# Optimization experiments

Measured on AMD Instinct MI355X. Metric: run time of the kernel, lower is better.

## Reference

```python
import jax, jax.numpy as jnp
import numpy as np

N_NODES = 100000
N_EDGES = 1600000
N_GRAPHS = 256
K_HOPS = 3


def setup_inputs() -> dict:
    key = jax.random.key(0)
    ks = jax.random.split(key, 10)
    x = jax.random.normal(ks[0], (N_NODES, 32), dtype=jnp.float32)
    edge_index = jax.random.randint(ks[1], (2, N_EDGES), 0, N_NODES, dtype=jnp.int32)
    batch = jnp.sort(jax.random.randint(ks[2], (N_NODES,), 0, N_GRAPHS, dtype=jnp.int32))
    gcn_w = jax.random.normal(ks[3], (64, 32), dtype=jnp.float32) * 0.1
    gcn_b = jax.random.normal(ks[4], (64,), dtype=jnp.float32) * 0.1
    w1 = jax.random.normal(ks[5], (32, 64), dtype=jnp.float32) * 0.1
    b1 = jax.random.normal(ks[6], (32,), dtype=jnp.float32) * 0.1
    w2 = jax.random.normal(ks[7], (16, 32), dtype=jnp.float32) * 0.1
    b2 = jax.random.normal(ks[8], (16,), dtype=jnp.float32) * 0.1
    return {"x": x, "edge_index": edge_index, "batch": batch,
            "gcn_w": gcn_w, "gcn_b": gcn_b, "w1": w1, "b1": b1, "w2": w2, "b2": b2}


def reference(x, edge_index, batch, gcn_w, gcn_b, w1, b1, w2, b2):
    N = x.shape[0]
    src, dst = edge_index[0], edge_index[1]
    # GCN symmetric normalization with self-loops: deg = in-degree + 1
    deg = jax.ops.segment_sum(jnp.ones_like(src, dtype=x.dtype), dst, num_segments=N) + 1.0
    norm = deg ** -0.5  # [N]
    h = x
    for _ in range(K_HOPS):
        # edge message: norm[src] * h[src], scattered to dst, scaled by norm[dst];
        # self-loop contributes norm[i]^2 * h[i]
        msg = h[src] * norm[src][:, None]                     # [E, C]
        agg = jax.ops.segment_sum(msg, dst, num_segments=N)    # [N, C]
        h = norm[:, None] * agg + (norm * norm)[:, None] * h
    h = jax.nn.relu(h @ gcn_w.T + gcn_b)                       # [N, hidden]
    # global mean pool per graph
    counts = jax.ops.segment_sum(jnp.ones((N,), x.dtype), batch, num_segments=N_GRAPHS)
    sums = jax.ops.segment_sum(h, batch, num_segments=N_GRAPHS)
    h_avg = sums / jnp.maximum(counts, 1.0)[:, None]           # [G, hidden]
    # classifier (dropout = identity in eval)
    h1 = jax.nn.relu(h_avg @ w1.T + b1)
    logits = h1 @ w2.T + b2                                    # [G, nc]
    return logits
```

## Files before the change

### kernel.cpp

```cpp
#include <hip/hip_runtime.h>

constexpr int NW    = 391;
constexpr int CH    = 8192;
constexpr int CAP_B = 8192;
constexpr int CAP_C = 10240;

__device__ __forceinline__ unsigned bf16_rne(float x) {
    unsigned u = __float_as_uint(x);
    u += 0x7fffu + ((u >> 16) & 1u);
    return u >> 16;
}
__device__ __forceinline__ unsigned pack2(float even, float odd) {
    return bf16_rne(even) | (bf16_rne(odd) << 16);
}
__device__ __forceinline__ float lo_f(unsigned u) { return __uint_as_float(u << 16); }
__device__ __forceinline__ float hi_f(unsigned u) { return __uint_as_float(u & 0xffff0000u); }


__global__ __launch_bounds__(512) void k_bucket(const int* __restrict__ src,
                                                const int* __restrict__ dst, int E,
                                                int* __restrict__ wcur, int* __restrict__ packed) {
    __shared__ int h[256];
    __shared__ int base[256];
    int t = threadIdx.x;
    if (t < 256) h[t] = 0;
    __syncthreads();
    int b0 = blockIdx.x * CH;
    int cnt = min(CH, E - b0);
    if (cnt == CH) {
        const int4* d4 = (const int4*)(dst + b0);
        for (int i = t; i < CH / 4; i += 512) {
            int4 v = d4[i];
            atomicAdd(&h[v.x / NW], 1); atomicAdd(&h[v.y / NW], 1);
            atomicAdd(&h[v.z / NW], 1); atomicAdd(&h[v.w / NW], 1);
        }
    } else {
        for (int i = t; i < cnt; i += 512) atomicAdd(&h[dst[b0 + i] / NW], 1);
    }
    __syncthreads();
    if (t < 256) { base[t] = atomicAdd(&wcur[t], h[t]); h[t] = 0; }
    __syncthreads();
    if (cnt == CH) {
        const int4* d4 = (const int4*)(dst + b0);
        const int4* s4 = (const int4*)(src + b0);
        for (int i = t; i < CH / 4; i += 512) {
            int4 dv = d4[i];
            int4 sv = s4[i];
            int da[4] = {dv.x, dv.y, dv.z, dv.w};
            int sa[4] = {sv.x, sv.y, sv.z, sv.w};
#pragma unroll
            for (int j = 0; j < 4; ++j) {
                int w = da[j] / NW;
                int l = da[j] - w * NW;
                int r = atomicAdd(&h[w], 1);
                int pos = base[w] + r;
                if (pos < CAP_B) packed[w * CAP_B + pos] = (l << 17) | sa[j];
            }
        }
    } else {
        for (int i = t; i < cnt; i += 512) {
            int d = dst[b0 + i];
            int s = src[b0 + i];
            int w = d / NW;
            int l = d - w * NW;
            int r = atomicAdd(&h[w], 1);
            int pos = base[w] + r;
            if (pos < CAP_B) packed[w * CAP_B + pos] = (l << 17) | s;
        }
    }
}


__global__ __launch_bounds__(512) void k_window(const int* __restrict__ packed,
                                                const int* __restrict__ wcur,
                                                const float4* __restrict__ x4,
                                                float* __restrict__ norm,
                                                int2* __restrict__ rng,
                                                int* __restrict__ csr,
                                                uint2* __restrict__ hb, int N, int W) {
    __shared__ int hist[NW];
    __shared__ float snorm[NW];
    __shared__ int pend[NW];
    __shared__ int cur[NW];
    __shared__ int wpart[8];
    int t = threadIdx.x, w = blockIdx.x;
    int lo = w * NW, nwn = min(NW, N - lo);
    for (int i = t; i < NW; i += 512) hist[i] = 0;
    __syncthreads();
    int cnt = min(wcur[w], CAP_B);
    const int* pk = packed + (size_t)w * CAP_B;
    for (int e = t; e < cnt; e += 512) atomicAdd(&hist[pk[e] >> 17], 1);
    __syncthreads();
    int d = (t < nwn) ? hist[t] : 0;
    float nv = rsqrtf((float)(d + 1));
    if (t < nwn) { snorm[t] = nv; norm[lo + t] = nv; }
    int pd = (t < nwn) ? ((d + 7) & ~7) : 0;
    int lane = t & 63, wid = t >> 6;
    int v = pd;
#pragma unroll
    for (int s = 1; s < 64; s <<= 1) {
        int u = __shfl_up(v, s, 64);
        if (lane >= s) v += u;
    }
    if (lane == 63) wpart[wid] = v;
    __syncthreads();
    if (t < 8) {
        int z = wpart[t];
#pragma unroll
        for (int s = 1; s < 8; s <<= 1) {
            int u = __shfl_up(z, s, 8);
            if (t >= s) z += u;
        }
        wpart[t] = z;
    }
    __syncthreads();
    int incl = v + (wid ? wpart[wid - 1] : 0);
    int base = w * CAP_C;
    int cend = base + incl;
    if (t < nwn) {
        rng[lo + t] = make_int2(cend - pd, cend);
        pend[t] = cend;
        cur[t] = cend - pd;
    }
    if (w == W - 1 && t == 0) { norm[N] = 1.f; rng[N] = make_int2(0, 0); }
    __syncthreads();
    for (int e = t; e < cnt; e += 512) {
        int p = pk[e];
        int pos = atomicAdd(&cur[p >> 17], 1);
        csr[pos] = p & 0x1FFFF;
    }
    __syncthreads();
    if (t < nwn) {
        for (int pos = cur[t]; pos < pend[t]; ++pos) csr[pos] = N;
    }
    for (int idx = t; idx < nwn * 8; idx += 512) {
        int node = idx >> 3, q = idx & 7;
        float nn = snorm[node];
        float4 vx = x4[(size_t)(lo + node) * 8 + q];
        hb[(size_t)(lo + node) * 8 + q] =
            make_uint2(pack2(vx.x * nn, vx.y * nn), pack2(vx.z * nn, vx.w * nn));
    }
    if (w == W - 1 && t < 8) hb[(size_t)N * 8 + t] = make_uint2(0u, 0u);
}

__global__ void k_hop(const uint2* __restrict__ tab, const float* __restrict__ norm,
                      const int2* __restrict__ rng, const int* __restrict__ csr,
                      uint2* __restrict__ outb, int N) {
    int group = (blockIdx.x * blockDim.x + threadIdx.x) >> 3;
    int l = threadIdx.x & 7;
    if (group > N) return;
    uint2 sv = tab[(size_t)group * 8 + l];
    float ax = lo_f(sv.x), ay = hi_f(sv.x), az = lo_f(sv.y), aw = hi_f(sv.y);
    int2 be = rng[group];
    int k = be.x;
    for (; k + 16 <= be.y; k += 16) {
        int e0 = csr[k + l];
        int e1 = csr[k + 8 + l];
        uint2 u[16];
#pragma unroll
        for (int j = 0; j < 8; ++j) {
            int s = __shfl(e0, j, 8);
            u[j] = tab[(size_t)s * 8 + l];
        }
#pragma unroll
        for (int j = 0; j < 8; ++j) {
            int s = __shfl(e1, j, 8);
            u[8 + j] = tab[(size_t)s * 8 + l];
        }
#pragma unroll
        for (int j = 0; j < 16; ++j) {
            ax += lo_f(u[j].x); ay += hi_f(u[j].x);
            az += lo_f(u[j].y); aw += hi_f(u[j].y);
        }
    }
    if (k < be.y) {
        int e = csr[k + l];
        uint2 u[8];
#pragma unroll
        for (int j = 0; j < 8; ++j) {
            int s = __shfl(e, j, 8);
            u[j] = tab[(size_t)s * 8 + l];
        }
#pragma unroll
        for (int j = 0; j < 8; ++j) {
            ax += lo_f(u[j].x); ay += hi_f(u[j].x);
            az += lo_f(u[j].y); aw += hi_f(u[j].y);
        }
    }
    float n = norm[group];
    float sc = n * n;
    outb[(size_t)group * 8 + l] = make_uint2(pack2(ax * sc, ay * sc), pack2(az * sc, aw * sc));
}

__global__ __launch_bounds__(256) void k_hopfeat(const uint2* __restrict__ tab,
                                                 const float* __restrict__ norm,
                                                 const int2* __restrict__ rng,
                                                 const int* __restrict__ csr,
                                                 const float* __restrict__ gw,
                                                 const float* __restrict__ gb,
                                                 uint4* __restrict__ zb4, int N) {
    __shared__ float wT[32][64];
    __shared__ float bs[64];
    __shared__ float rows[32][33];
    int t = threadIdx.x;
    for (int i = t; i < 64 * 32; i += 256) { int c = i >> 5, k = i & 31; wT[k][c] = gw[i]; }
    if (t < 64) bs[t] = gb[t];
    int group = (blockIdx.x * 256 + t) >> 3;
    int l = t & 7;
    int node = t >> 3;
    float ax = 0.f, ay = 0.f, az = 0.f, aw = 0.f;
    if (group <= N) {
        uint2 sv = tab[(size_t)group * 8 + l];
        ax = lo_f(sv.x); ay = hi_f(sv.x); az = lo_f(sv.y); aw = hi_f(sv.y);
        int2 be = rng[group];
        int k = be.x;
        for (; k + 16 <= be.y; k += 16) {
            int e0 = csr[k + l];
            int e1 = csr[k + 8 + l];
            uint2 u[16];
#pragma unroll
            for (int j = 0; j < 8; ++j) {
                int s = __shfl(e0, j, 8);
                u[j] = tab[(size_t)s * 8 + l];
            }
#pragma unroll
            for (int j = 0; j < 8; ++j) {
                int s = __shfl(e1, j, 8);
                u[8 + j] = tab[(size_t)s * 8 + l];
            }
#pragma unroll
            for (int j = 0; j < 16; ++j) {
                ax += lo_f(u[j].x); ay += hi_f(u[j].x);
                az += lo_f(u[j].y); aw += hi_f(u[j].y);
            }
        }
        if (k < be.y) {
            int e = csr[k + l];
            uint2 u[8];
#pragma unroll
            for (int j = 0; j < 8; ++j) {
                int s = __shfl(e, j, 8);
                u[j] = tab[(size_t)s * 8 + l];
            }
#pragma unroll
            for (int j = 0; j < 8; ++j) {
                ax += lo_f(u[j].x); ay += hi_f(u[j].x);
                az += lo_f(u[j].y); aw += hi_f(u[j].y);
            }
        }
        float n = norm[group];
        ax *= n; ay *= n; az *= n; aw *= n;
    }
    rows[node][l * 4 + 0] = ax;
    rows[node][l * 4 + 1] = ay;
    rows[node][l * 4 + 2] = az;
    rows[node][l * 4 + 3] = aw;
    __syncthreads();
    if (group < N) {
        int c0 = l * 8;
        float o[8];
#pragma unroll
        for (int cc = 0; cc < 8; ++cc) {
            float d = bs[c0 + cc];
#pragma unroll
            for (int k = 0; k < 32; ++k) d += rows[node][k] * wT[k][c0 + cc];
            o[cc] = fmaxf(d, 0.f);
        }
        zb4[(size_t)group * 8 + l] =
            make_uint4(pack2(o[0], o[1]), pack2(o[2], o[3]), pack2(o[4], o[5]), pack2(o[6], o[7]));
    }
}


__global__ __launch_bounds__(256) void k_pool(const uint2* __restrict__ zb2,
                                              const int* __restrict__ batch, int N,
                                              const float* __restrict__ w1, const float* __restrict__ b1,
                                              const float* __restrict__ w2, const float* __restrict__ b2,
                                              float* __restrict__ out) {
    __shared__ float4 part[16][17];
    __shared__ float havg[64];
    __shared__ float h1s[32];
    __shared__ int se[2];
    int t = threadIdx.x, g = blockIdx.x;
    if (t < 2) {
        int target = g + t;
        int lo = 0, hi = N;
        while (lo < hi) { int mid = (lo + hi) >> 1; if (batch[mid] < target) lo = mid + 1; else hi = mid; }
        se[t] = lo;
    }
    __syncthreads();
    int start = se[0], end = se[1];
    int q = t & 15;
    int r = t >> 4;
    float4 acc = make_float4(0.f, 0.f, 0.f, 0.f);
    for (int n = start + r; n < end; n += 16) {
        uint2 v = zb2[(size_t)n * 16 + q];
        acc.x += lo_f(v.x); acc.y += hi_f(v.x); acc.z += lo_f(v.y); acc.w += hi_f(v.y);
    }
    part[r][q] = acc;
    __syncthreads();
#pragma unroll
    for (int s = 8; s > 0; s >>= 1) {
        if (r < s) {
            float4 a = part[r][q], b = part[r + s][q];
            a.x += b.x; a.y += b.y; a.z += b.z; a.w += b.w;
            part[r][q] = a;
        }
        __syncthreads();
    }
    if (t < 16) {
        int cnt = end - start;
        float inv = 1.f / (float)(cnt > 0 ? cnt : 1);
        float4 a = part[0][t];
        havg[t * 4] = a.x * inv; havg[t * 4 + 1] = a.y * inv;
        havg[t * 4 + 2] = a.z * inv; havg[t * 4 + 3] = a.w * inv;
    }
    __syncthreads();
    if (t < 32) {
        float d = b1[t];
#pragma unroll
        for (int k = 0; k < 64; ++k) d += havg[k] * w1[t * 64 + k];
        h1s[t] = fmaxf(d, 0.f);
    }
    __syncthreads();
    if (t < 16) {
        float d = b2[t];
#pragma unroll
        for (int j = 0; j < 32; ++j) d += h1s[j] * w2[t * 32 + j];
        out[g * 16 + t] = d;
    }
}


extern "C" void kernel_launch(void* const* d_in, const int* in_sizes, int n_in,
                              void* d_out, int out_size, void* d_ws, size_t ws_size,
                              hipStream_t stream) {
    const float* x     = (const float*)d_in[0];
    const int*   ei    = (const int*)d_in[1];
    const int*   batch = (const int*)d_in[2];
    const float* gw    = (const float*)d_in[3];
    const float* gb    = (const float*)d_in[4];
    const float* w1    = (const float*)d_in[5];
    const float* b1    = (const float*)d_in[6];
    const float* w2    = (const float*)d_in[7];
    const float* b2    = (const float*)d_in[8];
    float* out = (float*)d_out;

    int N = in_sizes[2];
    int E = in_sizes[1] / 2;
    int G = out_size / 16;
    const int* srcp = ei;
    const int* dstp = ei + E;

    int W  = (N + NW - 1) / NW;
    int NB = (E + CH - 1) / CH;

    char* ws = (char*)d_ws;
    size_t off = 0;
    auto alloc = [&](size_t bytes) -> void* {
        void* p = ws + off;
        off += (bytes + 255) & ~(size_t)255;
        return p;
    };
    int*   wcur   = (int*)alloc(256 * 4);
    int*   packed = (int*)alloc((size_t)W * CAP_B * 4);
    int*   csr    = (int*)alloc((size_t)W * CAP_C * 4);
    int2*  rng    = (int2*)alloc((size_t)(N + 1) * 8);
    float* norm   = (float*)alloc((size_t)(N + 1) * 4);
    uint2* hbA    = (uint2*)alloc((size_t)(N + 1) * 64);
    uint2* hbB    = (uint2*)alloc((size_t)(N + 1) * 64);
    unsigned* zbuf = (unsigned*)alloc((size_t)N * 64 * 2);

    hipMemsetAsync(wcur, 0, 256 * 4, stream);

    int pb = ((N + 1) * 8 + 255) / 256;

    k_bucket<<<NB, 512, 0, stream>>>(srcp, dstp, E, wcur, packed);
    k_window<<<W, 512, 0, stream>>>(packed, wcur, (const float4*)x, norm, rng, csr, hbA, N, W);

    k_hop<<<pb, 256, 0, stream>>>(hbA, norm, rng, csr, hbB, N);
    k_hop<<<pb, 256, 0, stream>>>(hbB, norm, rng, csr, hbA, N);
    k_hopfeat<<<pb, 256, 0, stream>>>(hbA, norm, rng, csr, gw, gb, (uint4*)zbuf, N);

    k_pool<<<G, 256, 0, stream>>>((const uint2*)zbuf, batch, N, w1, b1, w2, b2, out);
}
```

Before: 203.0 us.

## Fuse all GCN stages into one persistent cooperative kernel with grid syncs

Replaces the six separate kernel launches with a single cooperative persistent kernel that runs bucket, window/CSR build, two hops, hop+feature and pool phases separated by grid.sync, and keeps the multi-launch path as a fallback. Window size, chunk size and block size are halved (NW 196, 256 threads) so each window fits a 256-thread block and more windows give better load balance. The aim is to remove launch gaps and tail effects between the small stages. In exchange the grid is capped at 1024 blocks with grid-stride loops, which may reduce latency hiding in the gather-heavy hop phases, and grid barriers add their own cost.

```diff
diff --git a/kernel.cpp b/kernel.cpp
--- a/kernel.cpp
+++ b/kernel.cpp
@@ -1,9 +1,13 @@
 #include <hip/hip_runtime.h>
-
-constexpr int NW    = 391;
-constexpr int CH    = 8192;
-constexpr int CAP_B = 8192;
-constexpr int CAP_C = 10240;
+#include <hip/hip_cooperative_groups.h>
+
+namespace cg = cooperative_groups;
+
+constexpr int NW    = 196;
+constexpr int CH    = 3200;
+constexpr int CAP_B = 4096;
+constexpr int CAP_C = 5632;
+constexpr int NTHR  = 256;
 
 __device__ __forceinline__ unsigned bf16_rne(float x) {
     unsigned u = __float_as_uint(x);
@@ -16,202 +20,150 @@
 __device__ __forceinline__ float lo_f(unsigned u) { return __uint_as_float(u << 16); }
 __device__ __forceinline__ float hi_f(unsigned u) { return __uint_as_float(u & 0xffff0000u); }
 
-
-__global__ __launch_bounds__(512) void k_bucket(const int* __restrict__ src,
-                                                const int* __restrict__ dst, int E,
-                                                int* __restrict__ wcur, int* __restrict__ packed) {
-    __shared__ int h[256];
-    __shared__ int base[256];
+struct KParams {
+    const int* src; const int* dst; int E;
+    int* wcur; int* packed;
+    const float4* x4; float* norm; int2* rng; int* csr;
+    uint2* hbA; uint2* hbB; uint4* zb4;
+    const int* batch; const float* gw; const float* gb;
+    const float* w1; const float* b1; const float* w2; const float* b2;
+    float* out; int N; int W; int NB; int G;
+};
+
+union SharedU {
+    struct { int h[512]; int base[512]; } bk;
+    struct { int hist[NW]; float snorm[NW]; int pend[NW]; int cur[NW]; int wpart[8]; } wd;
+    struct { float wT[32][64]; float bs[64]; float rows[32][33]; } ft;
+    struct { float4 part[16][17]; float havg[64]; float h1s[32]; int se[2]; } pl;
+};
+
+__device__ void phase_bucket(const KParams& p, SharedU& su) {
     int t = threadIdx.x;
-    if (t < 256) h[t] = 0;
-    __syncthreads();
-    int b0 = blockIdx.x * CH;
-    int cnt = min(CH, E - b0);
-    if (cnt == CH) {
-        const int4* d4 = (const int4*)(dst + b0);
-        for (int i = t; i < CH / 4; i += 512) {
-            int4 v = d4[i];
-            atomicAdd(&h[v.x / NW], 1); atomicAdd(&h[v.y / NW], 1);
-            atomicAdd(&h[v.z / NW], 1); atomicAdd(&h[v.w / NW], 1);
-        }
-    } else {
-        for (int i = t; i < cnt; i += 512) atomicAdd(&h[dst[b0 + i] / NW], 1);
-    }
-    __syncthreads();
-    if (t < 256) { base[t] = atomicAdd(&wcur[t], h[t]); h[t] = 0; }
-    __syncthreads();
-    if (cnt == CH) {
-        const int4* d4 = (const int4*)(dst + b0);
-        const int4* s4 = (const int4*)(src + b0);
-        for (int i = t; i < CH / 4; i += 512) {
-            int4 dv = d4[i];
-            int4 sv = s4[i];
-            int da[4] = {dv.x, dv.y, dv.z, dv.w};
-            int sa[4] = {sv.x, sv.y, sv.z, sv.w};
-#pragma unroll
-            for (int j = 0; j < 4; ++j) {
-                int w = da[j] / NW;
-                int l = da[j] - w * NW;
-                int r = atomicAdd(&h[w], 1);
-                int pos = base[w] + r;
-                if (pos < CAP_B) packed[w * CAP_B + pos] = (l << 17) | sa[j];
-            }
-        }
-    } else {
-        for (int i = t; i < cnt; i += 512) {
-            int d = dst[b0 + i];
-            int s = src[b0 + i];
-            int w = d / NW;
-            int l = d - w * NW;
-            int r = atomicAdd(&h[w], 1);
-            int pos = base[w] + r;
-            if (pos < CAP_B) packed[w * CAP_B + pos] = (l << 17) | s;
-        }
-    }
-}
-
-
-__global__ __launch_bounds__(512) void k_window(const int* __restrict__ packed,
-                                                const int* __restrict__ wcur,
-                                                const float4* __restrict__ x4,
-                                                float* __restrict__ norm,
-                                                int2* __restrict__ rng,
-                                                int* __restrict__ csr,
-                                                uint2* __restrict__ hb, int N, int W) {
-    __shared__ int hist[NW];
-    __shared__ float snorm[NW];
-    __shared__ int pend[NW];
-    __shared__ int cur[NW];
-    __shared__ int wpart[8];
-    int t = threadIdx.x, w = blockIdx.x;
-    int lo = w * NW, nwn = min(NW, N - lo);
-    for (int i = t; i < NW; i += 512) hist[i] = 0;
-    __syncthreads();
-    int cnt = min(wcur[w], CAP_B);
-    const int* pk = packed + (size_t)w * CAP_B;
-    for (int e = t; e < cnt; e += 512) atomicAdd(&hist[pk[e] >> 17], 1);
-    __syncthreads();
-    int d = (t < nwn) ? hist[t] : 0;
-    float nv = rsqrtf((float)(d + 1));
-    if (t < nwn) { snorm[t] = nv; norm[lo + t] = nv; }
-    int pd = (t < nwn) ? ((d + 7) & ~7) : 0;
-    int lane = t & 63, wid = t >> 6;
-    int v = pd;
-#pragma unroll
-    for (int s = 1; s < 64; s <<= 1) {
-        int u = __shfl_up(v, s, 64);
-        if (lane >= s) v += u;
-    }
-    if (lane == 63) wpart[wid] = v;
-    __syncthreads();
-    if (t < 8) {
-        int z = wpart[t];
-#pragma unroll
-        for (int s = 1; s < 8; s <<= 1) {
-            int u = __shfl_up(z, s, 8);
-            if (t >= s) z += u;
-        }
-        wpart[t] = z;
-    }
-    __syncthreads();
-    int incl = v + (wid ? wpart[wid - 1] : 0);
-    int base = w * CAP_C;
-    int cend = base + incl;
-    if (t < nwn) {
-        rng[lo + t] = make_int2(cend - pd, cend);
-        pend[t] = cend;
-        cur[t] = cend - pd;
-    }
-    if (w == W - 1 && t == 0) { norm[N] = 1.f; rng[N] = make_int2(0, 0); }
-    __syncthreads();
-    for (int e = t; e < cnt; e += 512) {
-        int p = pk[e];
-        int pos = atomicAdd(&cur[p >> 17], 1);
-        csr[pos] = p & 0x1FFFF;
-    }
-    __syncthreads();
-    if (t < nwn) {
-        for (int pos = cur[t]; pos < pend[t]; ++pos) csr[pos] = N;
-    }
-    for (int idx = t; idx < nwn * 8; idx += 512) {
-        int node = idx >> 3, q = idx & 7;
-        float nn = snorm[node];
-        float4 vx = x4[(size_t)(lo + node) * 8 + q];
-        hb[(size_t)(lo + node) * 8 + q] =
-            make_uint2(pack2(vx.x * nn, vx.y * nn), pack2(vx.z * nn, vx.w * nn));
-    }
-    if (w == W - 1 && t < 8) hb[(size_t)N * 8 + t] = make_uint2(0u, 0u);
-}
-
-__global__ void k_hop(const uint2* __restrict__ tab, const float* __restrict__ norm,
-                      const int2* __restrict__ rng, const int* __restrict__ csr,
-                      uint2* __restrict__ outb, int N) {
-    int group = (blockIdx.x * blockDim.x + threadIdx.x) >> 3;
-    int l = threadIdx.x & 7;
-    if (group > N) return;
-    uint2 sv = tab[(size_t)group * 8 + l];
-    float ax = lo_f(sv.x), ay = hi_f(sv.x), az = lo_f(sv.y), aw = hi_f(sv.y);
-    int2 be = rng[group];
-    int k = be.x;
-    for (; k + 16 <= be.y; k += 16) {
-        int e0 = csr[k + l];
-        int e1 = csr[k + 8 + l];
-        uint2 u[16];
-#pragma unroll
-        for (int j = 0; j < 8; ++j) {
-            int s = __shfl(e0, j, 8);
-            u[j] = tab[(size_t)s * 8 + l];
-        }
-#pragma unroll
-        for (int j = 0; j < 8; ++j) {
-            int s = __shfl(e1, j, 8);
-            u[8 + j] = tab[(size_t)s * 8 + l];
-        }
-#pragma unroll
-        for (int j = 0; j < 16; ++j) {
-            ax += lo_f(u[j].x); ay += hi_f(u[j].x);
-            az += lo_f(u[j].y); aw += hi_f(u[j].y);
-        }
-    }
-    if (k < be.y) {
-        int e = csr[k + l];
-        uint2 u[8];
-#pragma unroll
-        for (int j = 0; j < 8; ++j) {
-            int s = __shfl(e, j, 8);
-            u[j] = tab[(size_t)s * 8 + l];
-        }
-#pragma unroll
-        for (int j = 0; j < 8; ++j) {
-            ax += lo_f(u[j].x); ay += hi_f(u[j].x);
-            az += lo_f(u[j].y); aw += hi_f(u[j].y);
-        }
-    }
-    float n = norm[group];
-    float sc = n * n;
-    outb[(size_t)group * 8 + l] = make_uint2(pack2(ax * sc, ay * sc), pack2(az * sc, aw * sc));
-}
-
-__global__ __launch_bounds__(256) void k_hopfeat(const uint2* __restrict__ tab,
-                                                 const float* __restrict__ norm,
-                                                 const int2* __restrict__ rng,
-                                                 const int* __restrict__ csr,
-                                                 const float* __restrict__ gw,
-                                                 const float* __restrict__ gb,
-                                                 uint4* __restrict__ zb4, int N) {
-    __shared__ float wT[32][64];
-    __shared__ float bs[64];
-    __shared__ float rows[32][33];
+    for (int c = blockIdx.x; c < p.NB; c += gridDim.x) {
+        for (int i = t; i < 512; i += NTHR) su.bk.h[i] = 0;
+        __syncthreads();
+        int b0 = c * CH;
+        int cnt = min(CH, p.E - b0);
+        if (cnt == CH) {
+            const int4* d4 = (const int4*)(p.dst + b0);
+            for (int i = t; i < CH / 4; i += NTHR) {
+                int4 v = d4[i];
+                atomicAdd(&su.bk.h[v.x / NW], 1); atomicAdd(&su.bk.h[v.y / NW], 1);
+                atomicAdd(&su.bk.h[v.z / NW], 1); atomicAdd(&su.bk.h[v.w / NW], 1);
+            }
+        } else {
+            for (int i = t; i < cnt; i += NTHR) atomicAdd(&su.bk.h[p.dst[b0 + i] / NW], 1);
+        }
+        __syncthreads();
+        for (int i = t; i < 512; i += NTHR) {
+            su.bk.base[i] = (i < p.W && su.bk.h[i] > 0) ? atomicAdd(&p.wcur[i], su.bk.h[i]) : 0;
+            su.bk.h[i] = 0;
+        }
+        __syncthreads();
+        if (cnt == CH) {
+            const int4* d4 = (const int4*)(p.dst + b0);
+            const int4* s4 = (const int4*)(p.src + b0);
+            for (int i = t; i < CH / 4; i += NTHR) {
+                int4 dv = d4[i];
+                int4 sv = s4[i];
+                int da[4] = {dv.x, dv.y, dv.z, dv.w};
+                int sa[4] = {sv.x, sv.y, sv.z, sv.w};
+#pragma unroll
+                for (int j = 0; j < 4; ++j) {
+                    int w = da[j] / NW;
+                    int l = da[j] - w * NW;
+                    int r = atomicAdd(&su.bk.h[w], 1);
+                    int pos = su.bk.base[w] + r;
+                    if (pos < CAP_B) p.packed[w * CAP_B + pos] = (l << 17) | sa[j];
+                }
+            }
+        } else {
+            for (int i = t; i < cnt; i += NTHR) {
+                int d = p.dst[b0 + i];
+                int s = p.src[b0 + i];
+                int w = d / NW;
+                int l = d - w * NW;
+                int r = atomicAdd(&su.bk.h[w], 1);
+                int pos = su.bk.base[w] + r;
+                if (pos < CAP_B) p.packed[w * CAP_B + pos] = (l << 17) | s;
+            }
+        }
+        __syncthreads();
+    }
+}
+
+__device__ void phase_window(const KParams& p, SharedU& su) {
     int t = threadIdx.x;
-    for (int i = t; i < 64 * 32; i += 256) { int c = i >> 5, k = i & 31; wT[k][c] = gw[i]; }
-    if (t < 64) bs[t] = gb[t];
-    int group = (blockIdx.x * 256 + t) >> 3;
-    int l = t & 7;
-    int node = t >> 3;
-    float ax = 0.f, ay = 0.f, az = 0.f, aw = 0.f;
-    if (group <= N) {
+    for (int w = blockIdx.x; w < p.W; w += gridDim.x) {
+        int lo = w * NW, nwn = min(NW, p.N - lo);
+        for (int i = t; i < NW; i += NTHR) su.wd.hist[i] = 0;
+        __syncthreads();
+        int cnt = min(p.wcur[w], CAP_B);
+        const int* pk = p.packed + (size_t)w * CAP_B;
+        for (int e = t; e < cnt; e += NTHR) atomicAdd(&su.wd.hist[pk[e] >> 17], 1);
+        __syncthreads();
+        int d = (t < nwn) ? su.wd.hist[t] : 0;
+        float nv = rsqrtf((float)(d + 1));
+        if (t < nwn) { su.wd.snorm[t] = nv; p.norm[lo + t] = nv; }
+        int pd = (t < nwn) ? ((d + 7) & ~7) : 0;
+        int lane = t & 63, wid = t >> 6;
+        int v = pd;
+#pragma unroll
+        for (int s = 1; s < 64; s <<= 1) {
+            int u = __shfl_up(v, s, 64);
+            if (lane >= s) v += u;
+        }
+        if (lane == 63) su.wd.wpart[wid] = v;
+        __syncthreads();
+        if (t < 4) {
+            int z = su.wd.wpart[t];
+#pragma unroll
+            for (int s = 1; s < 4; s <<= 1) {
+                int u = __shfl_up(z, s, 4);
+                if (t >= s) z += u;
+            }
+            su.wd.wpart[t] = z;
+        }
+        __syncthreads();
+        int incl = v + (wid ? su.wd.wpart[wid - 1] : 0);
+        int cend = w * CAP_C + incl;
+        if (t < nwn) {
+            p.rng[lo + t] = make_int2(cend - pd, cend);
+            su.wd.pend[t] = cend;
+            su.wd.cur[t] = cend - pd;
+        }
+        if (w == p.W - 1 && t == 0) { p.norm[p.N] = 1.f; p.rng[p.N] = make_int2(0, 0); }
+        __syncthreads();
+        for (int e = t; e < cnt; e += NTHR) {
+            int pp = pk[e];
+            int pos = atomicAdd(&su.wd.cur[pp >> 17], 1);
+            p.csr[pos] = pp & 0x1FFFF;
+        }
+        __syncthreads();
+        if (t < nwn) {
+            for (int pos = su.wd.cur[t]; pos < su.wd.pend[t]; ++pos) p.csr[pos] = p.N;
+        }
+        for (int idx = t; idx < nwn * 8; idx += NTHR) {
+            int node = idx >> 3, q = idx & 7;
+            float nn = su.wd.snorm[node];
+            float4 vx = p.x4[(size_t)(lo + node) * 8 + q];
+            p.hbA[(size_t)(lo + node) * 8 + q] =
+                make_uint2(pack2(vx.x * nn, vx.y * nn), pack2(vx.z * nn, vx.w * nn));
+        }
+        if (w == p.W - 1 && t < 8) p.hbA[(size_t)p.N * 8 + t] = make_uint2(0u, 0u);
+        __syncthreads();
+    }
+}
+
+__device__ void hop_phase(const uint2* __restrict__ tab, const float* __restrict__ norm,
+                          const int2* __restrict__ rng, const int* __restrict__ csr,
+                          uint2* __restrict__ outb, int N) {
+    int stride = gridDim.x * blockDim.x;
+    int total = (N + 1) * 8;
+    for (int idx = blockIdx.x * blockDim.x + threadIdx.x; idx < total; idx += stride) {
+        int group = idx >> 3, l = idx & 7;
         uint2 sv = tab[(size_t)group * 8 + l];
-        ax = lo_f(sv.x); ay = hi_f(sv.x); az = lo_f(sv.y); aw = hi_f(sv.y);
+        float ax = lo_f(sv.x), ay = hi_f(sv.x), az = lo_f(sv.y), aw = hi_f(sv.y);
         int2 be = rng[group];
         int k = be.x;
         for (; k + 16 <= be.y; k += 16) {
@@ -249,138 +201,229 @@
             }
         }
         float n = norm[group];
-        ax *= n; ay *= n; az *= n; aw *= n;
-    }
-    rows[node][l * 4 + 0] = ax;
-    rows[node][l * 4 + 1] = ay;
-    rows[node][l * 4 + 2] = az;
-    rows[node][l * 4 + 3] = aw;
-    __syncthreads();
-    if (group < N) {
-        int c0 = l * 8;
-        float o[8];
-#pragma unroll
-        for (int cc = 0; cc < 8; ++cc) {
-            float d = bs[c0 + cc];
-#pragma unroll
-            for (int k = 0; k < 32; ++k) d += rows[node][k] * wT[k][c0 + cc];
-            o[cc] = fmaxf(d, 0.f);
-        }
-        zb4[(size_t)group * 8 + l] =
-            make_uint4(pack2(o[0], o[1]), pack2(o[2], o[3]), pack2(o[4], o[5]), pack2(o[6], o[7]));
-    }
-}
-
-
-__global__ __launch_bounds__(256) void k_pool(const uint2* __restrict__ zb2,
-                                              const int* __restrict__ batch, int N,
-                                              const float* __restrict__ w1, const float* __restrict__ b1,
-                                              const float* __restrict__ w2, const float* __restrict__ b2,
-                                              float* __restrict__ out) {
-    __shared__ float4 part[16][17];
-    __shared__ float havg[64];
-    __shared__ float h1s[32];
-    __shared__ int se[2];
-    int t = threadIdx.x, g = blockIdx.x;
-    if (t < 2) {
-        int target = g + t;
-        int lo = 0, hi = N;
-        while (lo < hi) { int mid = (lo + hi) >> 1; if (batch[mid] < target) lo = mid + 1; else hi = mid; }
-        se[t] = lo;
-    }
-    __syncthreads();
-    int start = se[0], end = se[1];
-    int q = t & 15;
-    int r = t >> 4;
-    float4 acc = make_float4(0.f, 0.f, 0.f, 0.f);
-    for (int n = start + r; n < end; n += 16) {
-        uint2 v = zb2[(size_t)n * 16 + q];
-        acc.x += lo_f(v.x); acc.y += hi_f(v.x); acc.z += lo_f(v.y); acc.w += hi_f(v.y);
-    }
-    part[r][q] = acc;
-    __syncthreads();
-#pragma unroll
-    for (int s = 8; s > 0; s >>= 1) {
-        if (r < s) {
-            float4 a = part[r][q], b = part[r + s][q];
-            a.x += b.x; a.y += b.y; a.z += b.z; a.w += b.w;
-            part[r][q] = a;
-        }
-        __syncthreads();
-    }
-    if (t < 16) {
-        int cnt = end - start;
-        float inv = 1.f / (float)(cnt > 0 ? cnt : 1);
-        float4 a = part[0][t];
-        havg[t * 4] = a.x * inv; havg[t * 4 + 1] = a.y * inv;
-        havg[t * 4 + 2] = a.z * inv; havg[t * 4 + 3] = a.w * inv;
-    }
-    __syncthreads();
-    if (t < 32) {
-        float d = b1[t];
-#pragma unroll
-        for (int k = 0; k < 64; ++k) d += havg[k] * w1[t * 64 + k];
-        h1s[t] = fmaxf(d, 0.f);
-    }
-    __syncthreads();
-    if (t < 16) {
-        float d = b2[t];
-#pragma unroll
-        for (int j = 0; j < 32; ++j) d += h1s[j] * w2[t * 32 + j];
-        out[g * 16 + t] = d;
-    }
-}
+        float sc = n * n;
+        outb[(size_t)group * 8 + l] = make_uint2(pack2(ax * sc, ay * sc), pack2(az * sc, aw * sc));
+    }
+}
+
+__device__ void phase_hopfeat(const KParams& p, SharedU& su) {
+    int t = threadIdx.x;
+    for (int i = t; i < 64 * 32; i += NTHR) { int c = i >> 5, k = i & 31; su.ft.wT[k][c] = p.gw[i]; }
+    if (t < 64) su.ft.bs[t] = p.gb[t];
+    int stride = gridDim.x * blockDim.x;
+    int total = (p.N + 1) * 8;
+    int node = t >> 3, l = t & 7;
+    for (int base = blockIdx.x * blockDim.x; base < total; base += stride) {
+        int idx = base + t;
+        int group = idx >> 3;
+        float ax = 0.f, ay = 0.f, az = 0.f, aw = 0.f;
+        if (idx < total) {
+            uint2 sv = p.hbA[(size_t)group * 8 + l];
+            ax = lo_f(sv.x); ay = hi_f(sv.x); az = lo_f(sv.y); aw = hi_f(sv.y);
+            int2 be = p.rng[group];
+            int k = be.x;
+            for (; k + 16 <= be.y; k += 16) {
+                int e0 = p.csr[k + l];
+                int e1 = p.csr[k + 8 + l];
+                uint2 u[16];
+#pragma unroll
+                for (int j = 0; j < 8; ++j) {
+                    int s = __shfl(e0, j, 8);
+                    u[j] = p.hbA[(size_t)s * 8 + l];
+                }
+#pragma unroll
+                for (int j = 0; j < 8; ++j) {
+                    int s = __shfl(e1, j, 8);
+                    u[8 + j] = p.hbA[(size_t)s * 8 + l];
+                }
+#pragma unroll
+                for (int j = 0; j < 16; ++j) {
+                    ax += lo_f(u[j].x); ay += hi_f(u[j].x);
+                    az += lo_f(u[j].y); aw += hi_f(u[j].y);
+                }
+            }
+            if (k < be.y) {
+                int e = p.csr[k + l];
+                uint2 u[8];
+#pragma unroll
+                for (int j = 0; j < 8; ++j) {
+                    int s = __shfl(e, j, 8);
+                    u[j] = p.hbA[(size_t)s * 8 + l];
+                }
+#pragma unroll
+                for (int j = 0; j < 8; ++j) {
+                    ax += lo_f(u[j].x); ay += hi_f(u[j].x);
+                    az += lo_f(u[j].y); aw += hi_f(u[j].y);
+                }
+            }
+            float n = p.norm[group];
+            ax *= n; ay *= n; az *= n; aw *= n;
+        }
+        su.ft.rows[node][l * 4 + 0] = ax;
+        su.ft.rows[node][l * 4 + 1] = ay;
+        su.ft.rows[node][l * 4 + 2] = az;
+        su.ft.rows[node][l * 4 + 3] = aw;
+        __syncthreads();
+        if (idx < total && group < p.N) {
+            int c0 = l * 8;
+            float o[8];
+#pragma unroll
+            for (int cc = 0; cc < 8; ++cc) {
+                float dd = su.ft.bs[c0 + cc];
+#pragma unroll
+                for (int k = 0; k < 32; ++k) dd += su.ft.rows[node][k] * su.ft.wT[k][c0 + cc];
+                o[cc] = fmaxf(dd, 0.f);
+            }
+            p.zb4[(size_t)group * 8 + l] = make_uint4(pack2(o[0], o[1]), pack2(o[2], o[3]),
+                                                      pack2(o[4], o[5]), pack2(o[6], o[7]));
+        }
+        __syncthreads();
+    }
+}
+
+__device__ void phase_pool(const KParams& p, SharedU& su) {
+    int t = threadIdx.x;
+    const uint2* zb2 = (const uint2*)p.zb4;
+    for (int g = blockIdx.x; g < p.G; g += gridDim.x) {
+        if (t < 2) {
+            int target = g + t;
+            int lo = 0, hi = p.N;
+            while (lo < hi) { int mid = (lo + hi) >> 1; if (p.batch[mid] < target) lo = mid + 1; else hi = mid; }
+            su.pl.se[t] = lo;
+        }
+        __syncthreads();
+        int start = su.pl.se[0], end = su.pl.se[1];
+        int q = t & 15;
+        int r = t >> 4;
+        float4 acc = make_float4(0.f, 0.f, 0.f, 0.f);
+        for (int n = start + r; n < end; n += 16) {
+            uint2 v = zb2[(size_t)n * 16 + q];
+            acc.x += lo_f(v.x); acc.y += hi_f(v.x); acc.z += lo_f(v.y); acc.w += hi_f(v.y);
+        }
+        su.pl.part[r][q] = acc;
+        __syncthreads();
+#pragma unroll
+        for (int s = 8; s > 0; s >>= 1) {
+            if (r < s) {
+                float4 a = su.pl.part[r][q], b = su.pl.part[r + s][q];
+                a.x += b.x; a.y += b.y; a.z += b.z; a.w += b.w;
+                su.pl.part[r][q] = a;
+            }
+            __syncthreads();
+        }
+        if (t < 16) {
+            int cnt = end - start;
+            float inv = 1.f / (float)(cnt > 0 ? cnt : 1);
+            float4 a = su.pl.part[0][t];
+            su.pl.havg[t * 4] = a.x * inv; su.pl.havg[t * 4 + 1] = a.y * inv;
+            su.pl.havg[t * 4 + 2] = a.z * inv; su.pl.havg[t * 4 + 3] = a.w * inv;
+        }
+        __syncthreads();
+        if (t < 32) {
+            float d = p.b1[t];
+#pragma unroll
+            for (int k = 0; k < 64; ++k) d += su.pl.havg[k] * p.w1[t * 64 + k];
+            su.pl.h1s[t] = fmaxf(d, 0.f);
+        }
+        __syncthreads();
+        if (t < 16) {
+            float d = p.b2[t];
+#pragma unroll
+            for (int j = 0; j < 32; ++j) d += su.pl.h1s[j] * p.w2[t * 32 + j];
+            p.out[g * 16 + t] = d;
+        }
+        __syncthreads();
+    }
+}
+
+__global__ __launch_bounds__(NTHR, 4) void k_all(KParams p) {
+    __shared__ SharedU su;
+    cg::grid_group grid = cg::this_grid();
+    phase_bucket(p, su);
+    grid.sync();
+    phase_window(p, su);
+    grid.sync();
+    hop_phase(p.hbA, p.norm, p.rng, p.csr, p.hbB, p.N);
+    grid.sync();
+    hop_phase(p.hbB, p.norm, p.rng, p.csr, p.hbA, p.N);
+    grid.sync();
+    phase_hopfeat(p, su);
+    grid.sync();
+    phase_pool(p, su);
+}
+
+__global__ __launch_bounds__(NTHR) void k_bucket_w(KParams p)  { __shared__ SharedU su; phase_bucket(p, su); }
+__global__ __launch_bounds__(NTHR) void k_window_w(KParams p)  { __shared__ SharedU su; phase_window(p, su); }
+__global__ __launch_bounds__(NTHR) void k_hop_w(const uint2* tab, const float* norm, const int2* rng,
+                                                const int* csr, uint2* outb, int N) {
+    hop_phase(tab, norm, rng, csr, outb, N);
+}
+__global__ __launch_bounds__(NTHR) void k_hopfeat_w(KParams p) { __shared__ SharedU su; phase_hopfeat(p, su); }
+__global__ __launch_bounds__(NTHR) void k_pool_w(KParams p)    { __shared__ SharedU su; phase_pool(p, su); }
 
 
 extern "C" void kernel_launch(void* const* d_in, const int* in_sizes, int n_in,
                               void* d_out, int out_size, void* d_ws, size_t ws_size,
                               hipStream_t stream) {
-    const float* x     = (const float*)d_in[0];
-    const int*   ei    = (const int*)d_in[1];
-    const int*   batch = (const int*)d_in[2];
-    const float* gw    = (const float*)d_in[3];
-    const float* gb    = (const float*)d_in[4];
-    const float* w1    = (const float*)d_in[5];
-    const float* b1    = (const float*)d_in[6];
-    const float* w2    = (const float*)d_in[7];
-    const float* b2    = (const float*)d_in[8];
-    float* out = (float*)d_out;
-
-    int N = in_sizes[2];
-    int E = in_sizes[1] / 2;
-    int G = out_size / 16;
-    const int* srcp = ei;
-    const int* dstp = ei + E;
-
-    int W  = (N + NW - 1) / NW;
-    int NB = (E + CH - 1) / CH;
+    KParams p;
+    p.x4    = (const float4*)d_in[0];
+    const int* ei = (const int*)d_in[1];
+    p.batch = (const int*)d_in[2];
+    p.gw    = (const float*)d_in[3];
+    p.gb    = (const float*)d_in[4];
+    p.w1    = (const float*)d_in[5];
+    p.b1    = (const float*)d_in[6];
+    p.w2    = (const float*)d_in[7];
+    p.b2    = (const float*)d_in[8];
+    p.out   = (float*)d_out;
+
+    p.N = in_sizes[2];
+    p.E = in_sizes[1] / 2;
+    p.G = out_size / 16;
+    p.src = ei;
+    p.dst = ei + p.E;
+    p.W  = (p.N + NW - 1) / NW;
+    p.NB = (p.E + CH - 1) / CH;
 
     char* ws = (char*)d_ws;
     size_t off = 0;
     auto alloc = [&](size_t bytes) -> void* {
-        void* p = ws + off;
+        void* q = ws + off;
         off += (bytes + 255) & ~(size_t)255;
-        return p;
+        return q;
     };
-    int*   wcur   = (int*)alloc(256 * 4);
-    int*   packed = (int*)alloc((size_t)W * CAP_B * 4);
-    int*   csr    = (int*)alloc((size_t)W * CAP_C * 4);
-    int2*  rng    = (int2*)alloc((size_t)(N + 1) * 8);
-    float* norm   = (float*)alloc((size_t)(N + 1) * 4);
-    uint2* hbA    = (uint2*)alloc((size_t)(N + 1) * 64);
-    uint2* hbB    = (uint2*)alloc((size_t)(N + 1) * 64);
-    unsigned* zbuf = (unsigned*)alloc((size_t)N * 64 * 2);
-
-    hipMemsetAsync(wcur, 0, 256 * 4, stream);
-
-    int pb = ((N + 1) * 8 + 255) / 256;
-
-    k_bucket<<<NB, 512, 0, stream>>>(srcp, dstp, E, wcur, packed);
-    k_window<<<W, 512, 0, stream>>>(packed, wcur, (const float4*)x, norm, rng, csr, hbA, N, W);
-
-    k_hop<<<pb, 256, 0, stream>>>(hbA, norm, rng, csr, hbB, N);
-    k_hop<<<pb, 256, 0, stream>>>(hbB, norm, rng, csr, hbA, N);
-    k_hopfeat<<<pb, 256, 0, stream>>>(hbA, norm, rng, csr, gw, gb, (uint4*)zbuf, N);
-
-    k_pool<<<G, 256, 0, stream>>>((const uint2*)zbuf, batch, N, w1, b1, w2, b2, out);
-}
+    p.wcur   = (int*)alloc(512 * 4);
+    p.packed = (int*)alloc((size_t)p.W * CAP_B * 4);
+    p.csr    = (int*)alloc((size_t)p.W * CAP_C * 4);
+    p.rng    = (int2*)alloc((size_t)(p.N + 1) * 8);
+    p.norm   = (float*)alloc((size_t)(p.N + 1) * 4);
+    p.hbA    = (uint2*)alloc((size_t)(p.N + 1) * 64);
+    p.hbB    = (uint2*)alloc((size_t)(p.N + 1) * 64);
+    p.zb4    = (uint4*)alloc((size_t)p.N * 64 * 2);
+
+    hipMemsetAsync(p.wcur, 0, 512 * 4, stream);
+
+    bool done = false;
+    int occ = 0;
+    hipError_t e = hipOccupancyMaxActiveBlocksPerMultiprocessor(&occ, (const void*)k_all, NTHR, 0);
+    if (e == hipSuccess && occ > 0) {
+        int grid = occ * 256;
+        if (grid > 1024) grid = 1024;
+        void* args[] = { &p };
+        e = hipLaunchCooperativeKernel((const void*)k_all, dim3(grid), dim3(NTHR), args, 0, stream);
+        if (e == hipSuccess) done = true;
+        else (void)hipGetLastError();
+    } else {
+        (void)hipGetLastError();
+    }
+
+    if (!done) {
+        int pb = ((p.N + 1) * 8 + NTHR - 1) / NTHR;
+        k_bucket_w<<<p.NB, NTHR, 0, stream>>>(p);
+        k_window_w<<<p.W, NTHR, 0, stream>>>(p);
+        k_hop_w<<<pb, NTHR, 0, stream>>>(p.hbA, p.norm, p.rng, p.csr, p.hbB, p.N);
+        k_hop_w<<<pb, NTHR, 0, stream>>>(p.hbB, p.norm, p.rng, p.csr, p.hbA, p.N);
+        k_hopfeat_w<<<1024, NTHR, 0, stream>>>(p);
+        k_pool_w<<<p.G, NTHR, 0, stream>>>(p);
+    }
+}
```

After: 551.0 us. 171% more time.

## Fuse mean-pool sum into final hop kernel with atomics; shrink bucket chunk

Applied to the files above, without the earlier changes.

The final hop-plus-GCN-linear kernel now reduces its ReLU outputs per graph in shared memory and atomically adds them into a small per-graph sum buffer. This removes the bf16 write and re-read of the N×64 feature buffer and shrinks the pool kernel to a small head kernel. Pooled sums are now kept in fp32 rather than rounded through bf16, but the atomic accumulation order is nondeterministic. Separately, the bucket chunk size is reduced so more blocks are launched.

```diff
diff --git a/kernel.cpp b/kernel.cpp
--- a/kernel.cpp
+++ b/kernel.cpp
@@ -1,7 +1,7 @@
 #include <hip/hip_runtime.h>
 
 constexpr int NW    = 391;
-constexpr int CH    = 8192;
+constexpr int CH    = 6400;
 constexpr int CAP_B = 8192;
 constexpr int CAP_C = 10240;
 
@@ -196,12 +196,14 @@
                                                  const float* __restrict__ norm,
                                                  const int2* __restrict__ rng,
                                                  const int* __restrict__ csr,
+                                                 const int* __restrict__ batch,
                                                  const float* __restrict__ gw,
                                                  const float* __restrict__ gb,
-                                                 uint4* __restrict__ zb4, int N) {
+                                                 float* __restrict__ gsum, int N) {
     __shared__ float wT[32][64];
     __shared__ float bs[64];
     __shared__ float rows[32][33];
+    __shared__ float acc[64];
     int t = threadIdx.x;
     for (int i = t; i < 64 * 32; i += 256) { int c = i >> 5, k = i & 31; wT[k][c] = gw[i]; }
     if (t < 64) bs[t] = gb[t];
@@ -256,9 +258,11 @@
     rows[node][l * 4 + 2] = az;
     rows[node][l * 4 + 3] = aw;
     __syncthreads();
+    float o[8] = {0.f, 0.f, 0.f, 0.f, 0.f, 0.f, 0.f, 0.f};
+    int gmy = 0x7fffffff;
     if (group < N) {
+        gmy = batch[group];
         int c0 = l * 8;
-        float o[8];
 #pragma unroll
         for (int cc = 0; cc < 8; ++cc) {
             float d = bs[c0 + cc];
@@ -266,18 +270,33 @@
             for (int k = 0; k < 32; ++k) d += rows[node][k] * wT[k][c0 + cc];
             o[cc] = fmaxf(d, 0.f);
         }
-        zb4[(size_t)group * 8 + l] =
-            make_uint4(pack2(o[0], o[1]), pack2(o[2], o[3]), pack2(o[4], o[5]), pack2(o[6], o[7]));
-    }
-}
-
-
-__global__ __launch_bounds__(256) void k_pool(const uint2* __restrict__ zb2,
-                                              const int* __restrict__ batch, int N,
-                                              const float* __restrict__ w1, const float* __restrict__ b1,
-                                              const float* __restrict__ w2, const float* __restrict__ b2,
-                                              float* __restrict__ out) {
-    __shared__ float4 part[16][17];
+    }
+    int n0 = blockIdx.x * 32;
+    int g0 = batch[min(n0, N - 1)];
+    int g1 = batch[min(n0 + 31, N - 1)];
+    for (int g = g0; g <= g1; ++g) {
+        if (t < 64) acc[t] = 0.f;
+        __syncthreads();
+        if (gmy == g) {
+            float* a = &acc[l * 8];
+#pragma unroll
+            for (int cc = 0; cc < 8; ++cc) atomicAdd(&a[cc], o[cc]);
+        }
+        __syncthreads();
+        if (t < 64) {
+            float v = acc[t];
+            if (v != 0.f) atomicAdd(&gsum[(size_t)g * 64 + t], v);
+        }
+        __syncthreads();
+    }
+}
+
+
+__global__ __launch_bounds__(64) void k_head(const float* __restrict__ gsum,
+                                             const int* __restrict__ batch, int N,
+                                             const float* __restrict__ w1, const float* __restrict__ b1,
+                                             const float* __restrict__ w2, const float* __restrict__ b2,
+                                             float* __restrict__ out) {
     __shared__ float havg[64];
     __shared__ float h1s[32];
     __shared__ int se[2];
@@ -289,32 +308,9 @@
         se[t] = lo;
     }
     __syncthreads();
-    int start = se[0], end = se[1];
-    int q = t & 15;
-    int r = t >> 4;
-    float4 acc = make_float4(0.f, 0.f, 0.f, 0.f);
-    for (int n = start + r; n < end; n += 16) {
-        uint2 v = zb2[(size_t)n * 16 + q];
-        acc.x += lo_f(v.x); acc.y += hi_f(v.x); acc.z += lo_f(v.y); acc.w += hi_f(v.y);
-    }
-    part[r][q] = acc;
-    __syncthreads();
-#pragma unroll
-    for (int s = 8; s > 0; s >>= 1) {
-        if (r < s) {
-            float4 a = part[r][q], b = part[r + s][q];
-            a.x += b.x; a.y += b.y; a.z += b.z; a.w += b.w;
-            part[r][q] = a;
-        }
-        __syncthreads();
-    }
-    if (t < 16) {
-        int cnt = end - start;
-        float inv = 1.f / (float)(cnt > 0 ? cnt : 1);
-        float4 a = part[0][t];
-        havg[t * 4] = a.x * inv; havg[t * 4 + 1] = a.y * inv;
-        havg[t * 4 + 2] = a.z * inv; havg[t * 4 + 3] = a.w * inv;
-    }
+    int cnt = se[1] - se[0];
+    float inv = 1.f / (float)(cnt > 0 ? cnt : 1);
+    havg[t] = gsum[(size_t)g * 64 + t] * inv;
     __syncthreads();
     if (t < 32) {
         float d = b1[t];
@@ -369,9 +365,10 @@
     float* norm   = (float*)alloc((size_t)(N + 1) * 4);
     uint2* hbA    = (uint2*)alloc((size_t)(N + 1) * 64);
     uint2* hbB    = (uint2*)alloc((size_t)(N + 1) * 64);
-    unsigned* zbuf = (unsigned*)alloc((size_t)N * 64 * 2);
+    float* gsum   = (float*)alloc((size_t)G * 64 * 4);
 
     hipMemsetAsync(wcur, 0, 256 * 4, stream);
+    hipMemsetAsync(gsum, 0, (size_t)G * 64 * 4, stream);
 
     int pb = ((N + 1) * 8 + 255) / 256;
 
@@ -380,7 +377,7 @@
 
     k_hop<<<pb, 256, 0, stream>>>(hbA, norm, rng, csr, hbB, N);
     k_hop<<<pb, 256, 0, stream>>>(hbB, norm, rng, csr, hbA, N);
-    k_hopfeat<<<pb, 256, 0, stream>>>(hbA, norm, rng, csr, gw, gb, (uint4*)zbuf, N);
-
-    k_pool<<<G, 256, 0, stream>>>((const uint2*)zbuf, batch, N, w1, b1, w2, b2, out);
-}
+    k_hopfeat<<<pb, 256, 0, stream>>>(hbA, norm, rng, csr, batch, gw, gb, gsum, N);
+
+    k_head<<<G, 64, 0, stream>>>(gsum, batch, N, w1, b1, w2, b2, out);
+}
```

Result: slower. 230.5 us (+13.6%).
